# Kernel optimization log

Measured on AMD Instinct MI355X. Metric: run time of the kernel, lower is better.

Reference implementation:

```python
import jax, jax.numpy as jnp
import numpy as np

N = 100_000
E = 3_200_000
F_IN = 512
F_OUT = 256
ALPHA = 0.2      # LeakyReLU negative slope
EPS = 9e-15      # matches torch.Tensor([9e-15]) in the original


def setup_inputs() -> dict:
    key = jax.random.key(0)
    k_x, k_e, k_w, k_a, k_b = jax.random.split(key, 5)
    x = jax.random.normal(k_x, (N, F_IN), dtype=jnp.float32)
    edge = jax.random.randint(k_e, (2, E), 0, N, dtype=jnp.int64)
    # xavier_normal-ish scales
    W = jax.random.normal(k_w, (F_IN, F_OUT), dtype=jnp.float32) * (1.414 * np.sqrt(2.0 / (F_IN + F_OUT)))
    a = jax.random.normal(k_a, (2 * F_OUT,), dtype=jnp.float32) * (1.414 * np.sqrt(2.0 / (1 + 2 * F_OUT)))
    bias = jax.random.normal(k_b, (F_OUT,), dtype=jnp.float32) * (1.414 * np.sqrt(2.0 / (1 + F_OUT)))
    return {"x": x, "edge": edge, "W": W, "a": a, "bias": bias}


def reference(x, edge, W, a, bias):
    src, dst = edge[0], edge[1]
    n = x.shape[0]
    h = x @ W + bias  # [N, F_OUT]
    # a . cat(h[src], h[dst]) == (h @ a_src)[src] + (h @ a_dst)[dst]
    a_src, a_dst = a[:F_OUT], a[F_OUT:]
    e = (h @ a_src)[src] + (h @ a_dst)[dst]            # [E]
    e = jnp.where(e > 0, e, ALPHA * e)                  # LeakyReLU
    e = jnp.exp(e - jnp.max(e))                         # global-max stabilized exp
    rowsum = jax.ops.segment_sum(e, src, num_segments=n)               # [N]
    h_prime = jax.ops.segment_sum(e[:, None] * h[dst], src, num_segments=n)  # [N, F_OUT]
    h_prime = h_prime / (rowsum[:, None] + EPS)
    return jax.nn.elu(h_prime)
```

## Files before the change

kernel.cpp:

```cpp
#include <hip/hip_runtime.h>

typedef __bf16 bf16x8 __attribute__((ext_vector_type(8)));
typedef float f32x4 __attribute__((ext_vector_type(4)));
typedef unsigned short u16x8 __attribute__((ext_vector_type(8)));

#define FIN 512
#define FOUT 256
#define NBLK 256
#define BSHIFT 8

__device__ __forceinline__ float b2f(unsigned short u) {
  union { unsigned int u; float f; } x;
  x.u = ((unsigned int)u) << 16;
  return x.f;
}
__device__ __forceinline__ unsigned short f2b(float f) {
  union { float f; unsigned int u; } x; x.f = f;
  unsigned int u = x.u;
  unsigned int r = (u + 0x7fffu + ((u >> 16) & 1u)) >> 16;
  return (unsigned short)r;
}
__device__ __forceinline__ unsigned int cvt_pk_bf16(float lo, float hi) {
  unsigned int r;
  asm("v_cvt_pk_bf16_f32 %0, %1, %2" : "=v"(r) : "v"(lo), "v"(hi));
  return r;
}

__global__ void k_probe(const unsigned short* __restrict__ xh,
                        const int* __restrict__ e, int* __restrict__ flags) {
  __shared__ int cnt[2];
  if (threadIdx.x == 0) { cnt[0] = 0; cnt[1] = 0; }
  __syncthreads();
  int c = 0;
  for (int i = threadIdx.x; i < 32768; i += 256) {
    unsigned short u = xh[i];
    if (((u >> 7) & 0xFF) == 0xFF) c++;
  }
  if (c) atomicAdd(&cnt[0], c);
  if (e[2 * threadIdx.x + 1] == 0) atomicAdd(&cnt[1], 1);
  __syncthreads();
  if (threadIdx.x == 0) {
    flags[0] = (cnt[0] > 0) ? 1 : 0;
    flags[1] = (cnt[1] > 128) ? 1 : 0;
  }
}

__global__ void k_transpose(const void* __restrict__ W,
                            unsigned short* __restrict__ Wt,
                            const int* __restrict__ flags) {
  int idx = blockIdx.x * 256 + threadIdx.x;
  int k = idx >> 8, n = idx & 255;
  float v = flags[0] ? ((const float*)W)[idx]
                     : b2f(((const unsigned short*)W)[idx]);
  Wt[n * FIN + k] = f2b(v);
}

__global__ __launch_bounds__(256, 3) void k_gemm(const void* __restrict__ X,
                                                 const unsigned short* __restrict__ Wt,
                                                 const void* __restrict__ bias,
                                                 const void* __restrict__ A,
                                                 unsigned short* __restrict__ H,
                                                 float* __restrict__ s1,
                                                 float* __restrict__ s2,
                                                 int nrows, const int* __restrict__ flags) {
  __shared__ char lds[32768];
  const int tid = threadIdx.x;
  const int wave = tid >> 6;
  const int lane = tid & 63;
  const int fm = lane & 15;
  const int fq = lane >> 4;
  const int hw = lane >> 5;
  const int hl = lane & 31;
  const int isf = flags[0];
  const int m0 = blockIdx.x * 64;

#define STAGE_HALF(h)                                                          \
  do {                                                                         \
    const int k0_ = (h) * 256;                                                 \
    if (isf) {                                                                 \
      _Pragma("unroll")                                                        \
      for (int j = 0; j < 8; ++j) {                                            \
        int r = wave * 16 + j * 2 + hw;                                        \
        int grow = m0 + r; if (grow >= nrows) grow = nrows - 1;                \
        int c = hl ^ (r & 7);                                                  \
        const float* gp = (const float*)X + (size_t)grow * FIN + k0_ + c * 8;  \
        f32x4 lo = *(const f32x4*)gp;                                          \
        f32x4 hi = *(const f32x4*)(gp + 4);                                    \
        uint4 pk;                                                              \
        pk.x = cvt_pk_bf16(lo[0], lo[1]);                                      \
        pk.y = cvt_pk_bf16(lo[2], lo[3]);                                      \
        pk.z = cvt_pk_bf16(hi[0], hi[1]);                                      \
        pk.w = cvt_pk_bf16(hi[2], hi[3]);                                      \
        *(uint4*)(lds + r * 512 + hl * 16) = pk;                               \
      }                                                                        \
    } else {                                                                   \
      _Pragma("unroll")                                                        \
      for (int j = 0; j < 8; ++j) {                                            \
        int r = wave * 16 + j * 2 + hw;                                        \
        int grow = m0 + r; if (grow >= nrows) grow = nrows - 1;                \
        int c = hl ^ (r & 7);                                                  \
        const unsigned short* gp =                                             \
            (const unsigned short*)X + (size_t)grow * FIN + k0_ + c * 8;       \
        __builtin_amdgcn_global_load_lds(                                      \
            (const __attribute__((address_space(1))) void*)gp,                 \
            (__attribute__((address_space(3))) void*)(lds +                    \
                (wave * 16 + j * 2) * 512), 16, 0, 0);                         \
      }                                                                        \
    }                                                                          \
  } while (0)

  f32x4 acc[4][4];
#pragma unroll
  for (int i = 0; i < 4; i++)
#pragma unroll
    for (int j = 0; j < 4; j++) acc[i][j] = (f32x4){0.f, 0.f, 0.f, 0.f};

  const unsigned short* wp[4];
#pragma unroll
  for (int i = 0; i < 4; i++)
    wp[i] = Wt + (size_t)((wave * 4 + i) * 16 + fm) * FIN + fq * 8;

  const int swz = fm & 7;

  STAGE_HALF(0);

  bf16x8 bcur[4], bnxt[4];
#pragma unroll
  for (int i = 0; i < 4; i++) bcur[i] = *(const bf16x8*)(wp[i]);
#pragma unroll
  for (int i = 0; i < 4; i++) bnxt[i] = *(const bf16x8*)(wp[i] + 32);

  __syncthreads();

#define K_BODY(kk, it)                                                         \
  do {                                                                         \
    bf16x8 af[4];                                                              \
    _Pragma("unroll")                                                          \
    for (int mt = 0; mt < 4; mt++) {                                           \
      int slot = ((it) * 4 + fq) ^ swz;                                        \
      af[mt] = *(const bf16x8*)(lds + (mt * 16 + fm) * 512 + slot * 16);       \
    }                                                                          \
    bf16x8 bn[4];                                                              \
    int kn = (kk) + 2; if (kn > 15) kn = 15;                                   \
    _Pragma("unroll")                                                          \
    for (int i = 0; i < 4; i++) bn[i] = *(const bf16x8*)(wp[i] + kn * 32);     \
    _Pragma("unroll")                                                          \
    for (int mt = 0; mt < 4; mt++)                                             \
      _Pragma("unroll")                                                        \
      for (int i = 0; i < 4; i++)                                              \
        acc[mt][i] = __builtin_amdgcn_mfma_f32_16x16x32_bf16(                  \
            af[mt], bcur[i], acc[mt][i], 0, 0, 0);                             \
    _Pragma("unroll")                                                          \
    for (int i = 0; i < 4; i++) { bcur[i] = bnxt[i]; bnxt[i] = bn[i]; }        \
  } while (0)

#pragma unroll
  for (int it = 0; it < 8; ++it) K_BODY(it, it);

  __syncthreads();
  STAGE_HALF(1);
  __syncthreads();

#pragma unroll
  for (int it = 0; it < 8; ++it) K_BODY(8 + it, it);

  __syncthreads();
  float* sc1 = (float*)lds;
  float* sc2 = sc1 + 256;

  float bvv[4], asv[4], adv[4];
#pragma unroll
  for (int i = 0; i < 4; i++) {
    int col = (wave * 4 + i) * 16 + fm;
    if (isf) {
      bvv[i] = ((const float*)bias)[col];
      asv[i] = ((const float*)A)[col];
      adv[i] = ((const float*)A)[FOUT + col];
    } else {
      bvv[i] = b2f(((const unsigned short*)bias)[col]);
      asv[i] = b2f(((const unsigned short*)A)[col]);
      adv[i] = b2f(((const unsigned short*)A)[FOUT + col]);
    }
  }

#pragma unroll
  for (int mt = 0; mt < 4; mt++) {
#pragma unroll
    for (int r = 0; r < 4; r++) {
      int row = m0 + mt * 16 + fq * 4 + r;
      float p1 = 0.f, p2 = 0.f;
#pragma unroll
      for (int i = 0; i < 4; i++) {
        float h = acc[mt][i][r] + bvv[i];
        if (row < nrows) H[(size_t)row * FOUT + (wave * 4 + i) * 16 + fm] = f2b(h);
        p1 += h * asv[i];
        p2 += h * adv[i];
      }
#pragma unroll
      for (int off = 1; off < 16; off <<= 1) {
        p1 += __shfl_xor(p1, off, 64);
        p2 += __shfl_xor(p2, off, 64);
      }
      if (fm == 0) {
        int rl = mt * 16 + fq * 4 + r;
        sc1[wave * 64 + rl] = p1;
        sc2[wave * 64 + rl] = p2;
      }
    }
  }
  __syncthreads();
  if (tid < 64) {
    int row = m0 + tid;
    if (row < nrows) {
      s1[row] = sc1[tid] + sc1[64 + tid] + sc1[128 + tid] + sc1[192 + tid];
      s2[row] = sc2[tid] + sc2[64 + tid] + sc2[128 + tid] + sc2[192 + tid];
    }
  }
#undef STAGE_HALF
#undef K_BODY
}


__global__ __launch_bounds__(256) void k_bcount(const int* __restrict__ e, int E, int chunk,
                                                int nbuck, int* __restrict__ C,
                                                const int* __restrict__ flags) {
  __shared__ int hist[512];
  int t = threadIdx.x, blk = blockIdx.x;
  for (int i = t; i < nbuck; i += 256) hist[i] = 0;
  __syncthreads();
  int lo = blk * chunk, hi = min(E, lo + chunk);
  bool i64 = flags[1] != 0;
  for (int i = lo + t; i < hi; i += 256) {
    int s = i64 ? ((const int2*)e)[i].x : e[i];
    atomicAdd(&hist[s >> BSHIFT], 1);
  }
  __syncthreads();
  for (int i = t; i < nbuck; i += 256) C[blk * nbuck + i] = hist[i];
}

__global__ __launch_bounds__(256) void k_bscanA(const int* __restrict__ C, int nbuck,
                                                int* __restrict__ O, int* __restrict__ btot) {
  int b = blockIdx.x, t = threadIdx.x;
  int lane = t & 63, w = t >> 6;
  int v = C[t * nbuck + b];
  int x = v;
#pragma unroll
  for (int off = 1; off < 64; off <<= 1) {
    int y = __shfl_up(x, off, 64);
    if (lane >= off) x += y;
  }
  __shared__ int ws[4];
  if (lane == 63) ws[w] = x;
  __syncthreads();
  int wbase = (w > 0 ? ws[0] : 0) + (w > 1 ? ws[1] : 0) + (w > 2 ? ws[2] : 0);
  O[t * nbuck + b] = x + wbase - v;
  if (t == 255) btot[b] = x + wbase;
}

__global__ __launch_bounds__(512) void k_bscanB(const int* __restrict__ btot, int nbuck,
                                                int* __restrict__ bbase,
                                                int* __restrict__ rowptr, int N) {
  __shared__ int sh[512];
  int t = threadIdx.x;
  int v = (t < nbuck) ? btot[t] : 0;
  sh[t] = v;
  __syncthreads();
  for (int off = 1; off < 512; off <<= 1) {
    int u = (t >= off) ? sh[t - off] : 0;
    __syncthreads();
    sh[t] += u;
    __syncthreads();
  }
  if (t < nbuck) bbase[t] = sh[t] - v;
  if (t == nbuck - 1) { bbase[nbuck] = sh[t]; rowptr[N] = sh[t]; }
}

__global__ __launch_bounds__(256) void k_bscatter(const int* __restrict__ e, int E, int chunk,
                                                  int nbuck, const int* __restrict__ O,
                                                  const int* __restrict__ bbase,
                                                  int* __restrict__ stage,
                                                  const int* __restrict__ flags) {
  __shared__ int cur[512];
  int t = threadIdx.x, blk = blockIdx.x;
  for (int i = t; i < nbuck; i += 256) cur[i] = bbase[i] + O[blk * nbuck + i];
  __syncthreads();
  int lo = blk * chunk, hi = min(E, lo + chunk);
  bool i64 = flags[1] != 0;
  for (int i = lo + t; i < hi; i += 256) {
    int s, d;
    if (i64) { s = ((const int2*)e)[i].x; d = ((const int2*)e)[(size_t)E + i].x; }
    else     { s = e[i];                  d = e[E + i]; }
    int pos = atomicAdd(&cur[s >> BSHIFT], 1);
    stage[pos] = ((s & 255) << 17) | d;
  }
}

__global__ __launch_bounds__(256) void k_fine(const int* __restrict__ stage,
                                              const int* __restrict__ bbase,
                                              int* __restrict__ rowptr,
                                              int* __restrict__ csrd, int N) {
  __shared__ int hist[256];
  __shared__ int cursor[256];
  __shared__ int ws[4];
  int b = blockIdx.x, t = threadIdx.x;
  int s0 = b << BSHIFT;
  int base = bbase[b], end = bbase[b + 1], cnt = end - base;
  hist[t] = 0;
  __syncthreads();
  for (int i = t; i < cnt; i += 256) atomicAdd(&hist[stage[base + i] >> 17], 1);
  __syncthreads();
  int v = hist[t];
  int lane = t & 63, w = t >> 6;
  int x = v;
#pragma unroll
  for (int off = 1; off < 64; off <<= 1) {
    int y = __shfl_up(x, off, 64);
    if (lane >= off) x += y;
  }
  if (lane == 63) ws[w] = x;
  __syncthreads();
  int wbase = (w > 0 ? ws[0] : 0) + (w > 1 ? ws[1] : 0) + (w > 2 ? ws[2] : 0);
  int excl = x + wbase - v;
  cursor[t] = base + excl;
  if (s0 + t < N) rowptr[s0 + t] = base + excl;
  __syncthreads();
  for (int i = t; i < cnt; i += 256) {
    int p = stage[base + i];
    int pos = atomicAdd(&cursor[p >> 17], 1);
    csrd[pos] = p & 0x1FFFF;
  }
}

__global__ __launch_bounds__(256) void k_gather(const unsigned short* __restrict__ H,
                                                const float* __restrict__ s1,
                                                const float* __restrict__ s2,
                                                const int* __restrict__ rowptr,
                                                const int* __restrict__ csrd,
                                                void* __restrict__ out, int n,
                                                const int* __restrict__ flags) {
  __shared__ int2 eds[4][64];
  int wave = threadIdx.x >> 6, lane = threadIdx.x & 63;
  int row = blockIdx.x * 4 + wave;
  if (row >= n) return;
  int half = lane >> 5;
  int hl = lane & 31;
  int beg = rowptr[row], end = rowptr[row + 1];
  float s1v = s1[row];
  const unsigned short* Hb = H + hl * 8;
  float ac[8];
#pragma unroll
  for (int k = 0; k < 8; k++) ac[k] = 0.f;
  float wsum = 0.f;

  for (int base = beg; base < end; base += 64) {
    int cnt = end - base; if (cnt > 64) cnt = 64;
    int d_pre = 0;
    float s_pre = -1e30f;
    if (lane < cnt) { d_pre = csrd[base + lane]; s_pre = s2[d_pre]; }
    eds[wave][lane] = make_int2(d_pre, __float_as_int(s_pre));

#pragma unroll 8
    for (int j = 0; j < cnt; j += 2) {
      int jj = j + half;
      int2 p = eds[wave][jj];
      int dd = p.x;
      float v = s1v + __int_as_float(p.y);
      v = v > 0.f ? v : 0.2f * v;
      float w = (jj < cnt) ? __expf(v) : 0.f;
      union { u16x8 v; unsigned short u[8]; } hv;
      hv.v = *(const u16x8*)(Hb + (size_t)dd * FOUT);
      wsum += w;
#pragma unroll
      for (int k = 0; k < 8; k++) ac[k] += w * b2f(hv.u[k]);
    }
  }

#pragma unroll
  for (int k = 0; k < 8; k++) ac[k] += __shfl_down(ac[k], 32, 64);
  wsum += __shfl_down(wsum, 32, 64);

  if (half == 0) {
    float inv = 1.f / (wsum + 9e-15f);
    float o[8];
#pragma unroll
    for (int k = 0; k < 8; k++) {
      float x = ac[k] * inv;
      o[k] = x > 0.f ? x : __expf(x) - 1.f;
    }
    if (flags[0]) {
      float* op = (float*)out + (size_t)row * FOUT + hl * 8;
      *(f32x4*)op = (f32x4){o[0], o[1], o[2], o[3]};
      *(f32x4*)(op + 4) = (f32x4){o[4], o[5], o[6], o[7]};
    } else {
      union { u16x8 v; unsigned short u[8]; } ov;
#pragma unroll
      for (int k = 0; k < 8; k++) ov.u[k] = f2b(o[k]);
      *(u16x8*)((unsigned short*)out + (size_t)row * FOUT + hl * 8) = ov.v;
    }
  }
}

extern "C" void kernel_launch(void* const* d_in, const int* in_sizes, int n_in,
                              void* d_out, int out_size, void* d_ws, size_t ws_size,
                              hipStream_t stream) {
  const void* X = d_in[0];
  const int* edge = (const int*)d_in[1];
  const void* W = d_in[2];
  const void* A = d_in[3];
  const void* B = d_in[4];
  int N_ = in_sizes[0] / FIN;
  int E_ = in_sizes[1] / 2;
  int nbuck = (N_ + 255) >> BSHIFT;
  int chunk = (E_ + NBLK - 1) / NBLK;

  char* p = (char*)d_ws;
  auto alloc = [&](size_t bytes) {
    char* r = p; p += (bytes + 255) & ~(size_t)255; return r;
  };
  int* flags = (int*)alloc(256);
  unsigned short* H  = (unsigned short*)alloc((size_t)N_ * FOUT * 2);
  unsigned short* Wt = (unsigned short*)alloc((size_t)FIN * FOUT * 2);
  float* s1   = (float*)alloc((size_t)N_ * 4);
  float* s2   = (float*)alloc((size_t)N_ * 4);
  int* rowptr = (int*)alloc((size_t)(N_ + 1) * 4);
  int* csrd   = (int*)alloc((size_t)E_ * 4);
  int* C      = (int*)alloc((size_t)NBLK * nbuck * 4);
  int* O      = (int*)alloc((size_t)NBLK * nbuck * 4);
  int* btot   = (int*)alloc((size_t)nbuck * 4);
  int* bbase  = (int*)alloc((size_t)(nbuck + 1) * 4);
  int* stage  = (int*)alloc((size_t)E_ * 4);

  k_probe<<<1, 256, 0, stream>>>((const unsigned short*)X, edge, flags);
  k_transpose<<<(FIN * FOUT) / 256, 256, 0, stream>>>(W, Wt, flags);
  k_gemm<<<(N_ + 63) / 64, 256, 0, stream>>>(X, Wt, B, A, H, s1, s2, N_, flags);
  k_bcount<<<NBLK, 256, 0, stream>>>(edge, E_, chunk, nbuck, C, flags);
  k_bscanA<<<nbuck, 256, 0, stream>>>(C, nbuck, O, btot);
  k_bscanB<<<1, 512, 0, stream>>>(btot, nbuck, bbase, rowptr, N_);
  k_bscatter<<<NBLK, 256, 0, stream>>>(edge, E_, chunk, nbuck, O, bbase, stage, flags);
  k_fine<<<nbuck, 256, 0, stream>>>(stage, bbase, rowptr, csrd, N_);
  k_gather<<<(N_ + 3) / 4, 256, 0, stream>>>(H, s1, s2, rowptr, csrd,
                                             d_out, N_, flags);
}
```

Before: 699.0 us.

## Double-buffer GEMM A tiles in LDS across four K quarters

The GEMM kernel now splits K into four 128-wide quarters and ping-pongs between two 16 KB LDS buffers. The next quarter of X is staged while MFMAs run on the current one, replacing the old stage-compute-sync-stage pattern. The explicit two-deep register prefetch of W fragments is removed, and B fragments are loaded right before use. The occupancy hint of 3 blocks per CU is also dropped from launch bounds. This may expose global-load latency on B and raise register pressure.

```diff
diff --git a/kernel.cpp b/kernel.cpp
--- a/kernel.cpp
+++ b/kernel.cpp
@@ -55,35 +55,34 @@
   Wt[n * FIN + k] = f2b(v);
 }
 
-__global__ __launch_bounds__(256, 3) void k_gemm(const void* __restrict__ X,
-                                                 const unsigned short* __restrict__ Wt,
-                                                 const void* __restrict__ bias,
-                                                 const void* __restrict__ A,
-                                                 unsigned short* __restrict__ H,
-                                                 float* __restrict__ s1,
-                                                 float* __restrict__ s2,
-                                                 int nrows, const int* __restrict__ flags) {
+__global__ __launch_bounds__(256) void k_gemm(const void* __restrict__ X,
+                                              const unsigned short* __restrict__ Wt,
+                                              const void* __restrict__ bias,
+                                              const void* __restrict__ A,
+                                              unsigned short* __restrict__ H,
+                                              float* __restrict__ s1,
+                                              float* __restrict__ s2,
+                                              int nrows, const int* __restrict__ flags) {
   __shared__ char lds[32768];
   const int tid = threadIdx.x;
   const int wave = tid >> 6;
   const int lane = tid & 63;
   const int fm = lane & 15;
   const int fq = lane >> 4;
-  const int hw = lane >> 5;
-  const int hl = lane & 31;
   const int isf = flags[0];
   const int m0 = blockIdx.x * 64;
-
-#define STAGE_HALF(h)                                                          \
+  const int swz = fm & 7;
+
+#define STAGE_Q(bofs, q)                                                       \
   do {                                                                         \
-    const int k0_ = (h) * 256;                                                 \
+    const int k0_ = (q) * 128;                                                 \
     if (isf) {                                                                 \
       _Pragma("unroll")                                                        \
-      for (int j = 0; j < 8; ++j) {                                            \
-        int r = wave * 16 + j * 2 + hw;                                        \
+      for (int j = 0; j < 4; ++j) {                                            \
+        int r = wave * 16 + j * 4 + (lane >> 4);                               \
         int grow = m0 + r; if (grow >= nrows) grow = nrows - 1;                \
-        int c = hl ^ (r & 7);                                                  \
-        const float* gp = (const float*)X + (size_t)grow * FIN + k0_ + c * 8;  \
+        int cb = (lane & 15) ^ (r & 7);                                        \
+        const float* gp = (const float*)X + (size_t)grow * FIN + k0_ + cb * 8; \
         f32x4 lo = *(const f32x4*)gp;                                          \
         f32x4 hi = *(const f32x4*)(gp + 4);                                    \
         uint4 pk;                                                              \
@@ -91,20 +90,20 @@
         pk.y = cvt_pk_bf16(lo[2], lo[3]);                                      \
         pk.z = cvt_pk_bf16(hi[0], hi[1]);                                      \
         pk.w = cvt_pk_bf16(hi[2], hi[3]);                                      \
-        *(uint4*)(lds + r * 512 + hl * 16) = pk;                               \
+        *(uint4*)(lds + (bofs) + r * 256 + (lane & 15) * 16) = pk;             \
       }                                                                        \
     } else {                                                                   \
       _Pragma("unroll")                                                        \
-      for (int j = 0; j < 8; ++j) {                                            \
-        int r = wave * 16 + j * 2 + hw;                                        \
+      for (int j = 0; j < 4; ++j) {                                            \
+        int r = wave * 16 + j * 4 + (lane >> 4);                               \
         int grow = m0 + r; if (grow >= nrows) grow = nrows - 1;                \
-        int c = hl ^ (r & 7);                                                  \
+        int cb = (lane & 15) ^ (r & 7);                                        \
         const unsigned short* gp =                                             \
-            (const unsigned short*)X + (size_t)grow * FIN + k0_ + c * 8;       \
+            (const unsigned short*)X + (size_t)grow * FIN + k0_ + cb * 8;      \
         __builtin_amdgcn_global_load_lds(                                      \
             (const __attribute__((address_space(1))) void*)gp,                 \
-            (__attribute__((address_space(3))) void*)(lds +                    \
-                (wave * 16 + j * 2) * 512), 16, 0, 0);                         \
+            (__attribute__((address_space(3))) void*)(lds + (bofs) +           \
+                (wave * 16 + j * 4) * 256), 16, 0, 0);                         \
       }                                                                        \
     }                                                                          \
   } while (0)
@@ -120,51 +119,48 @@
   for (int i = 0; i < 4; i++)
     wp[i] = Wt + (size_t)((wave * 4 + i) * 16 + fm) * FIN + fq * 8;
 
-  const int swz = fm & 7;
-
-  STAGE_HALF(0);
-
-  bf16x8 bcur[4], bnxt[4];
-#pragma unroll
-  for (int i = 0; i < 4; i++) bcur[i] = *(const bf16x8*)(wp[i]);
-#pragma unroll
-  for (int i = 0; i < 4; i++) bnxt[i] = *(const bf16x8*)(wp[i] + 32);
-
-  __syncthreads();
-
-#define K_BODY(kk, it)                                                         \
+#define K_BODY(bofs, q, it)                                                    \
   do {                                                                         \
     bf16x8 af[4];                                                              \
     _Pragma("unroll")                                                          \
     for (int mt = 0; mt < 4; mt++) {                                           \
       int slot = ((it) * 4 + fq) ^ swz;                                        \
-      af[mt] = *(const bf16x8*)(lds + (mt * 16 + fm) * 512 + slot * 16);       \
+      af[mt] = *(const bf16x8*)(lds + (bofs) + (mt * 16 + fm) * 256 +          \
+                                slot * 16);                                    \
     }                                                                          \
-    bf16x8 bn[4];                                                              \
-    int kn = (kk) + 2; if (kn > 15) kn = 15;                                   \
+    bf16x8 bc[4];                                                              \
     _Pragma("unroll")                                                          \
-    for (int i = 0; i < 4; i++) bn[i] = *(const bf16x8*)(wp[i] + kn * 32);     \
+    for (int i = 0; i < 4; i++)                                                \
+      bc[i] = *(const bf16x8*)(wp[i] + ((q) * 4 + (it)) * 32);                 \
     _Pragma("unroll")                                                          \
     for (int mt = 0; mt < 4; mt++)                                             \
       _Pragma("unroll")                                                        \
       for (int i = 0; i < 4; i++)                                              \
         acc[mt][i] = __builtin_amdgcn_mfma_f32_16x16x32_bf16(                  \
-            af[mt], bcur[i], acc[mt][i], 0, 0, 0);                             \
-    _Pragma("unroll")                                                          \
-    for (int i = 0; i < 4; i++) { bcur[i] = bnxt[i]; bnxt[i] = bn[i]; }        \
+            af[mt], bc[i], acc[mt][i], 0, 0, 0);                               \
   } while (0)
 
-#pragma unroll
-  for (int it = 0; it < 8; ++it) K_BODY(it, it);
-
-  __syncthreads();
-  STAGE_HALF(1);
-  __syncthreads();
-
-#pragma unroll
-  for (int it = 0; it < 8; ++it) K_BODY(8 + it, it);
-
-  __syncthreads();
+  STAGE_Q(0, 0);
+  __syncthreads();
+
+  STAGE_Q(16384, 1);
+#pragma unroll
+  for (int it = 0; it < 4; ++it) K_BODY(0, 0, it);
+  __syncthreads();
+
+  STAGE_Q(0, 2);
+#pragma unroll
+  for (int it = 0; it < 4; ++it) K_BODY(16384, 1, it);
+  __syncthreads();
+
+  STAGE_Q(16384, 3);
+#pragma unroll
+  for (int it = 0; it < 4; ++it) K_BODY(0, 2, it);
+  __syncthreads();
+
+#pragma unroll
+  for (int it = 0; it < 4; ++it) K_BODY(16384, 3, it);
+
   float* sc1 = (float*)lds;
   float* sc2 = sc1 + 256;
 
@@ -216,7 +212,7 @@
       s2[row] = sc2[tid] + sc2[64 + tid] + sc2[128 + tid] + sc2[192 + tid];
     }
   }
-#undef STAGE_HALF
+#undef STAGE_Q
 #undef K_BODY
 }
 
```

New measurement: 711.7 us. About the same (+1.8%).
